# Kernel tuning notes

Hardware: AMD Instinct MI355X
Metric: run time of the kernel (lower is better)

## Reference

```python
import jax, jax.numpy as jnp
import numpy as np

N_NODES = 50000
N_EDGES = 1600000
F_IN = 128
C = 64          # block in/out channels
EF = 64         # edge MLP hidden dim
BLOCKS = 3
MLP_DIM = 128
N_CLASSES = 10
N_GRAPHS = 512
EPS = 1e-5


def setup_inputs() -> dict:
    key = jax.random.key(0)
    ks = jax.random.split(key, 32)
    s = 0.05
    inp = {
        "x": jax.random.normal(ks[0], (N_NODES, F_IN), jnp.float32),
        "edge_index": jax.random.randint(ks[1], (2, N_EDGES), 0, N_NODES, jnp.int64),
        "batch": jnp.sort(jax.random.randint(ks[2], (N_NODES,), 0, N_GRAPHS, jnp.int64)),
        "fc0_w": jax.random.normal(ks[3], (F_IN, C), jnp.float32) * s,
        "fc0_b": jnp.zeros((C,), jnp.float32),
        "fc1_w": jax.random.normal(ks[4], (BLOCKS * C, MLP_DIM), jnp.float32) * s,
        "fc1_b": jnp.zeros((MLP_DIM,), jnp.float32),
        "fc2_w": jax.random.normal(ks[5], (MLP_DIM, N_CLASSES), jnp.float32) * s,
        "fc2_b": jnp.zeros((N_CLASSES,), jnp.float32),
    }
    for i in range(BLOCKS):
        k = 6 + 4 * i
        inp[f"bn_g{i}"] = jnp.ones((C,), jnp.float32)
        inp[f"bn_b{i}"] = jnp.zeros((C,), jnp.float32)
        inp[f"w1_{i}"] = jax.random.normal(ks[k], (2 * C, EF), jnp.float32) * s
        inp[f"b1_{i}"] = jnp.zeros((EF,), jnp.float32)
        inp[f"w2_{i}"] = jax.random.normal(ks[k + 1], (EF, C), jnp.float32) * s
        inp[f"b2_{i}"] = jnp.zeros((C,), jnp.float32)
    return inp


def _batchnorm(x, g, b):
    mu = jnp.mean(x, axis=0)
    var = jnp.var(x, axis=0)
    return (x - mu) * jax.lax.rsqrt(var + EPS) * g + b


def _edge_conv(x, src, dst, w1, b1, w2, b2):
    # PyG-style EdgeConv: msg = MLP(concat[x_i, x_j - x_i]), max-aggregate at i
    xi = x[dst]                                  # [E, C]
    xj = x[src]                                  # [E, C]
    h = jax.nn.relu(jnp.concatenate([xi, xj - xi], axis=-1) @ w1 + b1)  # [E, EF]
    m = h @ w2 + b2                              # [E, C]
    agg = jax.ops.segment_max(m, dst, num_segments=N_NODES)
    return jnp.where(jnp.isfinite(agg), agg, 0.0)


def reference(x, edge_index, batch, fc0_w, fc0_b, fc1_w, fc1_b, fc2_w, fc2_b,
              bn_g0, bn_b0, w1_0, b1_0, w2_0, b2_0,
              bn_g1, bn_b1, w1_1, b1_1, w2_1, b2_1,
              bn_g2, bn_b2, w1_2, b1_2, w2_2, b2_2):
    src, dst = edge_index[0], edge_index[1]
    h = x @ fc0_w + fc0_b                        # [N, C]
    blocks = [(bn_g0, bn_b0, w1_0, b1_0, w2_0, b2_0),
              (bn_g1, bn_b1, w1_1, b1_1, w2_1, b2_1),
              (bn_g2, bn_b2, w1_2, b1_2, w2_2, b2_2)]
    xs = []
    for (g, b, w1, b1, w2, b2) in blocks:
        h = _batchnorm(h, g, b)
        h = jax.nn.relu(_edge_conv(h, src, dst, w1, b1, w2, b2))
        xs.append(h)
    cat = jnp.concatenate(xs, axis=-1)           # [N, 3C]
    # global mean pool over graphs
    sums = jax.ops.segment_sum(cat, batch, num_segments=N_GRAPHS)
    cnt = jax.ops.segment_sum(jnp.ones((N_NODES,), cat.dtype), batch,
                              num_segments=N_GRAPHS)
    pooled = sums / jnp.maximum(cnt, 1.0)[:, None]   # [G, 3C]
    hid = jax.nn.relu(pooled @ fc1_w + fc1_b)
    return jax.nn.log_softmax(hid @ fc2_w + fc2_b, axis=-1)
```

## Files before the change

### kernel.cpp

```cpp
#include <hip/hip_runtime.h>
#include <math.h>

#define N_NODES 50000
#define N_TILES 3125
#define N_EDGES 1600000
#define F_IN 128
#define C 64
#define EF 64
#define N_GRAPHS 512
#define MLP_DIM 128
#define N_CLASSES 10
#define EPS 1e-5f
#define NB 196
#define CAPB 16384
#define CHUNK 4096
#define NPASS1 391
#define NFC0 782
#define NSLICE 8
#define EDGE_GRID 2048

typedef __attribute__((ext_vector_type(8))) _Float16 half8;
typedef __attribute__((ext_vector_type(2))) _Float16 half2v;
typedef __attribute__((ext_vector_type(4))) float floatx4;
typedef __attribute__((ext_vector_type(4))) unsigned uintx4;

union Uh { uintx4 v; half2v h[4]; half8 h8; };

__device__ __forceinline__ unsigned short f2h(float a) {
    union { _Float16 f; unsigned short u; } c;
    c.f = (_Float16)a;
    return c.u;
}
__device__ __forceinline__ float h2f(unsigned short u) {
    union { unsigned short u; _Float16 f; } c;
    c.u = u;
    return (float)c.f;
}
__device__ __forceinline__ half2v pk2(float a, float b) {
    auto t = __builtin_amdgcn_cvt_pkrtz(a, b);
    union { decltype(t) i; half2v o; } c;
    c.i = t;
    return c.o;
}

__global__ __launch_bounds__(256, 3) void fc0_pass1_kernel(
        const int* __restrict__ src, const int* __restrict__ dst,
        int* __restrict__ gcur, unsigned* __restrict__ keys,
        const float* __restrict__ x, const float* __restrict__ w,
        const float* __restrict__ b, unsigned short* __restrict__ h0,
        float* __restrict__ bns) {
    __shared__ int lcnt[NB], lbase[NB], lcnt2[NB];
    __shared__ float bl1[4][64], bl2[4][64];
    int tid = threadIdx.x;

    if (blockIdx.x < NPASS1) {
        int e0 = blockIdx.x * CHUNK;
        unsigned k[CHUNK / 256];
        int bk[CHUNK / 256];
        for (int i = tid; i < NB; i += 256) lcnt[i] = 0;
        __syncthreads();
#pragma unroll
        for (int i = 0; i < CHUNK / 256; i++) {
            int e = e0 + i * 256 + tid;
            if (e < N_EDGES) {
                int d = dst[e];
                k[i] = ((unsigned)d << 16) | (unsigned)src[e];
                bk[i] = d >> 8;
                atomicAdd(&lcnt[bk[i]], 1);
            } else bk[i] = -1;
        }
        __syncthreads();
        for (int i = tid; i < NB; i += 256) {
            int c = lcnt[i];
            lbase[i] = c ? atomicAdd(&gcur[i], c) : 0;
            lcnt2[i] = 0;
        }
        __syncthreads();
#pragma unroll
        for (int i = 0; i < CHUNK / 256; i++) {
            if (bk[i] >= 0) {
                int r = atomicAdd(&lcnt2[bk[i]], 1);
                keys[(size_t)bk[i] * CAPB + lbase[bk[i]] + r] = k[i];
            }
        }
        return;
    }

    int bid = blockIdx.x - NPASS1;
    int lane = tid & 63, wid = tid >> 6;
    int q = lane >> 4, cl = lane & 15, kq = q * 8;

    Uh wf[4][4];
#pragma unroll
    for (int kh = 0; kh < 4; kh++)
#pragma unroll
        for (int cb = 0; cb < 4; cb++)
#pragma unroll
            for (int j = 0; j < 4; j++) {
                int k0 = kh * 32 + kq + 2 * j;
                int col = cb * 16 + cl;
                wf[kh][cb].h[j] = pk2(w[k0 * 64 + col], w[(k0 + 1) * 64 + col]);
            }
    float bv[4];
#pragma unroll
    for (int cb = 0; cb < 4; cb++) bv[cb] = b[cb * 16 + cl];
    float s1[4] = {0, 0, 0, 0}, s2[4] = {0, 0, 0, 0};

    for (int t = bid * 4 + wid; t < N_TILES; t += NFC0 * 4) {
        int nb = t * 16;
        floatx4 acc[4] = {{0,0,0,0},{0,0,0,0},{0,0,0,0},{0,0,0,0}};
#pragma unroll
        for (int kh = 0; kh < 4; kh++) {
            const float* xr = x + (size_t)(nb + cl) * F_IN + kh * 32 + kq;
            floatx4 xa = *(const floatx4*)xr;
            floatx4 xb = *(const floatx4*)(xr + 4);
            Uh xf;
            xf.h[0] = pk2(xa.x, xa.y); xf.h[1] = pk2(xa.z, xa.w);
            xf.h[2] = pk2(xb.x, xb.y); xf.h[3] = pk2(xb.z, xb.w);
#pragma unroll
            for (int cb = 0; cb < 4; cb++)
                acc[cb] = __builtin_amdgcn_mfma_f32_16x16x32_f16(xf.h8, wf[kh][cb].h8, acc[cb], 0, 0, 0);
        }
#pragma unroll
        for (int cb = 0; cb < 4; cb++)
#pragma unroll
            for (int r = 0; r < 4; r++) {
                float v = acc[cb][r] + bv[cb];
                h0[(size_t)(nb + q * 4 + r) * 64 + cb * 16 + cl] = f2h(v);
                s1[cb] += v; s2[cb] += v * v;
            }
    }
#pragma unroll
    for (int cb = 0; cb < 4; cb++) {
        s1[cb] += __shfl_xor(s1[cb], 16); s1[cb] += __shfl_xor(s1[cb], 32);
        s2[cb] += __shfl_xor(s2[cb], 16); s2[cb] += __shfl_xor(s2[cb], 32);
    }
    if (lane < 16) {
#pragma unroll
        for (int cb = 0; cb < 4; cb++) { bl1[wid][cb * 16 + lane] = s1[cb]; bl2[wid][cb * 16 + lane] = s2[cb]; }
    }
    __syncthreads();
    if (tid < 64) {
        float a  = bl1[0][tid] + bl1[1][tid] + bl1[2][tid] + bl1[3][tid];
        float c2 = bl2[0][tid] + bl2[1][tid] + bl2[2][tid] + bl2[3][tid];
        int sl = bid & (NSLICE - 1);
        atomicAdd(&bns[sl * 128 + tid], a);
        atomicAdd(&bns[sl * 128 + 64 + tid], c2);
    }
}

__device__ __forceinline__ void ab_body(int bid, int tid,
                                        const unsigned short* __restrict__ h,
                                        const float* __restrict__ bns,
                                        const float* __restrict__ g,
                                        const float* __restrict__ bb,
                                        const float* __restrict__ w1,
                                        const float* __restrict__ b1,
                                        unsigned short* __restrict__ A,
                                        unsigned short* __restrict__ Bb,
                                        float* scale, float* shift, float* cab) {
    int lane = tid & 63, wid = tid >> 6;
    int q = lane >> 4, cl = lane & 15, kq = q * 8;

    if (tid < 64) {
        float s1v = 0.f, s2v = 0.f;
#pragma unroll
        for (int s = 0; s < NSLICE; s++) { s1v += bns[s * 128 + tid]; s2v += bns[s * 128 + 64 + tid]; }
        float mu  = s1v * (1.0f / N_NODES);
        float var = s2v * (1.0f / N_NODES) - mu * mu;
        float sc  = g[tid] * rsqrtf(var + EPS);
        scale[tid] = sc;
        shift[tid] = bb[tid] - mu * sc;
    }
    __syncthreads();
    if (tid < 128) {
        int j = tid & 63;
        float acc = (tid < 64) ? b1[j] : 0.f;
        for (int k = 0; k < 64; k++) {
            float wa_ = w1[k * EF + j], wb_ = w1[(64 + k) * EF + j];
            acc = fmaf(shift[k], (tid < 64) ? (wa_ - wb_) : wb_, acc);
        }
        cab[tid] = acc;
    }
    Uh wa[2][4], wb[2][4];
#pragma unroll
    for (int kh = 0; kh < 2; kh++)
#pragma unroll
        for (int cb = 0; cb < 4; cb++)
#pragma unroll
            for (int j = 0; j < 4; j++) {
                int k0 = kh * 32 + kq + 2 * j;
                int col = cb * 16 + cl;
                float sa = scale[k0], sb = scale[k0 + 1];
                float a0 = w1[k0 * EF + col], b0 = w1[(64 + k0) * EF + col];
                float a1 = w1[(k0 + 1) * EF + col], b1v = w1[(64 + k0 + 1) * EF + col];
                wa[kh][cb].h[j] = pk2(sa * (a0 - b0), sb * (a1 - b1v));
                wb[kh][cb].h[j] = pk2(sa * b0, sb * b1v);
            }
    __syncthreads();
    float cav[4], cbv[4];
#pragma unroll
    for (int cb = 0; cb < 4; cb++) { cav[cb] = cab[cb * 16 + cl]; cbv[cb] = cab[64 + cb * 16 + cl]; }

    for (int t = bid * 4 + wid; t < N_TILES; t += NFC0 * 4) {
        int nb = t * 16;
        const unsigned short* hrow = h + (size_t)(nb + cl) * 64 + kq;
        Uh h0f, h1f;
        h0f.v = *(const uintx4*)hrow;
        h1f.v = *(const uintx4*)(hrow + 32);
        floatx4 accA[4] = {{0,0,0,0},{0,0,0,0},{0,0,0,0},{0,0,0,0}};
        floatx4 accB[4] = {{0,0,0,0},{0,0,0,0},{0,0,0,0},{0,0,0,0}};
#pragma unroll
        for (int cb = 0; cb < 4; cb++) {
            accA[cb] = __builtin_amdgcn_mfma_f32_16x16x32_f16(h0f.h8, wa[0][cb].h8, accA[cb], 0, 0, 0);
            accB[cb] = __builtin_amdgcn_mfma_f32_16x16x32_f16(h0f.h8, wb[0][cb].h8, accB[cb], 0, 0, 0);
            accA[cb] = __builtin_amdgcn_mfma_f32_16x16x32_f16(h1f.h8, wa[1][cb].h8, accA[cb], 0, 0, 0);
            accB[cb] = __builtin_amdgcn_mfma_f32_16x16x32_f16(h1f.h8, wb[1][cb].h8, accB[cb], 0, 0, 0);
        }
#pragma unroll
        for (int cb = 0; cb < 4; cb++)
#pragma unroll
            for (int r = 0; r < 4; r++) {
                size_t o = (size_t)(nb + q * 4 + r) * 64 + cb * 16 + cl;
                A[o]  = f2h(accA[cb][r] + cav[cb]);
                Bb[o] = f2h(accB[cb][r] + cbv[cb]);
            }
    }
}

__global__ __launch_bounds__(256, 4) void sort2_ab_kernel(
        const unsigned* __restrict__ keys, const int* __restrict__ bcnt,
        int* __restrict__ cnt, int* __restrict__ gtotal,
        int* __restrict__ row_start, unsigned short* __restrict__ sorted_src,
        const unsigned short* __restrict__ h, const float* __restrict__ bns,
        const float* __restrict__ g, const float* __restrict__ bb,
        const float* __restrict__ w1, const float* __restrict__ b1,
        unsigned short* __restrict__ A, unsigned short* __restrict__ Bb) {
    __shared__ int lc[256], loc[256], rs[256], cur[256];
    __shared__ int base;
    __shared__ float scale[64], shift[64], cab[128];
    int tid = threadIdx.x;
    if (blockIdx.x < NB) {
        int b = blockIdx.x;
        lc[tid] = 0;
        cur[tid] = 0;
        __syncthreads();
        int beg = b * CAPB, end = beg + bcnt[b];
        const unsigned* kb = keys + beg;
        int nk = end - beg;
        for (int p = tid; p < nk; p += 256)
            atomicAdd(&lc[(kb[p] >> 16) & 255], 1);
        __syncthreads();
        int node = b * 256 + tid;
        int c = lc[tid];
        if (node < N_NODES) cnt[node] = c;
        int pc = (c + 15) & ~15;
        loc[tid] = pc;
        __syncthreads();
        for (int off = 1; off < 256; off <<= 1) {
            int t = (tid >= off) ? loc[tid - off] : 0;
            __syncthreads();
            loc[tid] += t;
            __syncthreads();
        }
        if (tid == 255) base = atomicAdd(gtotal, loc[255]);
        __syncthreads();
        int myrs = base + loc[tid] - pc;
        rs[tid] = myrs;
        if (node < N_NODES) row_start[node] = myrs;
        __syncthreads();
        for (int p = tid; p < nk; p += 256) {
            unsigned k = kb[p];
            int lidx = (k >> 16) & 255;
            int r = atomicAdd(&cur[lidx], 1);
            sorted_src[rs[lidx] + r] = (unsigned short)(k & 0xFFFFu);
        }
        __syncthreads();
        if (node < N_NODES && c > 0) {
            unsigned short s0 = sorted_src[myrs];
            int pe = myrs + pc;
            for (int p = myrs + c; p < pe; p++) sorted_src[p] = s0;
        }
        return;
    }
    ab_body(blockIdx.x - NB, tid, h, bns, g, bb, w1, b1, A, Bb, scale, shift, cab);
}

__global__ __launch_bounds__(256, 4) void ab_mfma_kernel(
        const unsigned short* __restrict__ h, const float* __restrict__ bns,
        const float* __restrict__ g, const float* __restrict__ bb,
        const float* __restrict__ w1, const float* __restrict__ b1,
        unsigned short* __restrict__ A, unsigned short* __restrict__ Bb) {
    __shared__ float scale[64], shift[64], cab[128];
    ab_body(blockIdx.x, threadIdx.x, h, bns, g, bb, w1, b1, A, Bb, scale, shift, cab);
}

__global__ __launch_bounds__(256, 4) void edge_mfma_kernel(
        const unsigned short* __restrict__ A, const unsigned short* __restrict__ Bb,
        const int* __restrict__ row_start, const int* __restrict__ cnt,
        const unsigned short* __restrict__ sorted_src,
        const float* __restrict__ w2, const float* __restrict__ b2,
        unsigned short* __restrict__ catp, float* __restrict__ bnsNext) {
    __shared__ float r1[4][64], r2[4][64];
    int tid = threadIdx.x, lane = tid & 63, wid = tid >> 6;
    int kq = (lane >> 4) * 8;
    int cl = lane & 15;

    Uh bfr[2][4];
#pragma unroll
    for (int kh = 0; kh < 2; kh++)
#pragma unroll
        for (int cb = 0; cb < 4; cb++)
#pragma unroll
            for (int j = 0; j < 4; j++) {
                _Float16 w0 = (_Float16)w2[(kh * 32 + kq + 2 * j) * 64 + cb * 16 + cl];
                _Float16 w1v = (_Float16)w2[(kh * 32 + kq + 2 * j + 1) * 64 + cb * 16 + cl];
                bfr[kh][cb].h[j] = half2v{w0, w1v};
            }
    float b2j = b2[lane];
    float s1 = 0.f, s2 = 0.f;
    const half2v zeroh = {(_Float16)0.f, (_Float16)0.f};

    for (int n = blockIdx.x * 4 + wid; n < N_NODES; n += gridDim.x * 4) {
        int beg = row_start[n];
        int end = beg + ((cnt[n] + 15) & ~15);
        const unsigned short* arow = A + (size_t)n * 64 + kq;
        Uh a0u, a1u;
        a0u.v = __builtin_nontemporal_load((const uintx4*)(arow));
        a1u.v = __builtin_nontemporal_load((const uintx4*)(arow + 32));
        floatx4 rmax0 = {-INFINITY, -INFINITY, -INFINITY, -INFINITY};
        floatx4 rmax1 = rmax0, rmax2 = rmax0, rmax3 = rmax0;

        auto tile = [&](uintx4 u0, uintx4 u1) {
            Uh b0u, b1u, f0, f1;
            b0u.v = u0; b1u.v = u1;
#pragma unroll
            for (int j = 0; j < 4; j++) {
                f0.h[j] = __builtin_elementwise_max(a0u.h[j] + b0u.h[j], zeroh);
                f1.h[j] = __builtin_elementwise_max(a1u.h[j] + b1u.h[j], zeroh);
            }
            floatx4 acc0 = {0.f, 0.f, 0.f, 0.f}, acc1 = acc0, acc2 = acc0, acc3 = acc0;
            acc0 = __builtin_amdgcn_mfma_f32_16x16x32_f16(f0.h8, bfr[0][0].h8, acc0, 0, 0, 0);
            acc1 = __builtin_amdgcn_mfma_f32_16x16x32_f16(f0.h8, bfr[0][1].h8, acc1, 0, 0, 0);
            acc2 = __builtin_amdgcn_mfma_f32_16x16x32_f16(f0.h8, bfr[0][2].h8, acc2, 0, 0, 0);
            acc3 = __builtin_amdgcn_mfma_f32_16x16x32_f16(f0.h8, bfr[0][3].h8, acc3, 0, 0, 0);
            acc0 = __builtin_amdgcn_mfma_f32_16x16x32_f16(f1.h8, bfr[1][0].h8, acc0, 0, 0, 0);
            acc1 = __builtin_amdgcn_mfma_f32_16x16x32_f16(f1.h8, bfr[1][1].h8, acc1, 0, 0, 0);
            acc2 = __builtin_amdgcn_mfma_f32_16x16x32_f16(f1.h8, bfr[1][2].h8, acc2, 0, 0, 0);
            acc3 = __builtin_amdgcn_mfma_f32_16x16x32_f16(f1.h8, bfr[1][3].h8, acc3, 0, 0, 0);
            rmax0 = __builtin_elementwise_max(rmax0, acc0);
            rmax1 = __builtin_elementwise_max(rmax1, acc1);
            rmax2 = __builtin_elementwise_max(rmax2, acc2);
            rmax3 = __builtin_elementwise_max(rmax3, acc3);
        };
        auto gather = [&](int p, uintx4& u0, uintx4& u1) {
            int srcm = __builtin_nontemporal_load(&sorted_src[p + cl]);
            const unsigned short* brow = Bb + (size_t)srcm * 64 + kq;
            u0 = *(const uintx4*)(brow);
            u1 = *(const uintx4*)(brow + 32);
        };

        int p0 = beg;
        for (; p0 + 32 <= end; p0 += 32) {
            uintx4 x0, x1, y0, y1;
            gather(p0, x0, x1);
            gather(p0 + 16, y0, y1);
            tile(x0, x1);
            tile(y0, y1);
        }
        if (p0 < end) {
            uintx4 x0, x1;
            gather(p0, x0, x1);
            tile(x0, x1);
        }

        float v0 = fmaxf(fmaxf(rmax0.x, rmax0.y), fmaxf(rmax0.z, rmax0.w));
        float v1 = fmaxf(fmaxf(rmax1.x, rmax1.y), fmaxf(rmax1.z, rmax1.w));
        float v2 = fmaxf(fmaxf(rmax2.x, rmax2.y), fmaxf(rmax2.z, rmax2.w));
        float v3 = fmaxf(fmaxf(rmax3.x, rmax3.y), fmaxf(rmax3.z, rmax3.w));
        v0 = fmaxf(v0, __shfl_xor(v0, 16)); v0 = fmaxf(v0, __shfl_xor(v0, 32));
        v1 = fmaxf(v1, __shfl_xor(v1, 16)); v1 = fmaxf(v1, __shfl_xor(v1, 32));
        v2 = fmaxf(v2, __shfl_xor(v2, 16)); v2 = fmaxf(v2, __shfl_xor(v2, 32));
        v3 = fmaxf(v3, __shfl_xor(v3, 16)); v3 = fmaxf(v3, __shfl_xor(v3, 32));
        float vs = (lane & 32) ? ((lane & 16) ? v3 : v2) : ((lane & 16) ? v1 : v0);
        float v = fmaxf(vs + b2j, 0.f);
        __builtin_nontemporal_store(f2h(v), &catp[(size_t)n * 64 + lane]);
        s1 += v; s2 += v * v;
    }

    if (bnsNext) {
        r1[wid][lane] = s1; r2[wid][lane] = s2;
        __syncthreads();
        if (tid < 64) {
            float a  = r1[0][tid] + r1[1][tid] + r1[2][tid] + r1[3][tid];
            float c2 = r2[0][tid] + r2[1][tid] + r2[2][tid] + r2[3][tid];
            int sl = blockIdx.x & (NSLICE - 1);
            atomicAdd(&bnsNext[sl * 128 + tid], a);
            atomicAdd(&bnsNext[sl * 128 + 64 + tid], c2);
        }
    }
}

__global__ __launch_bounds__(192) void poolhead_kernel(const unsigned short* __restrict__ cat0,
                                                       const unsigned short* __restrict__ cat1,
                                                       const unsigned short* __restrict__ cat2,
                                                       const int* __restrict__ batch,
                                                       const float* __restrict__ fc1w,
                                                       const float* __restrict__ fc1b,
                                                       const float* __restrict__ fc2w,
                                                       const float* __restrict__ fc2b,
                                                       float* __restrict__ out) {
    __shared__ int se[2];
    __shared__ float p[192];
    __shared__ float hid[128];
    __shared__ float z[10];
    __shared__ float lse;
    int g = blockIdx.x, tid = threadIdx.x;
    if (tid < 2) {
        int target = g + tid;
        int lo = 0, hi = N_NODES;
        while (lo < hi) { int mid = (lo + hi) >> 1; if (batch[mid] < target) lo = mid + 1; else hi = mid; }
        se[tid] = lo;
    }
    __syncthreads();
    int s = se[0], e = se[1];
    const unsigned short* plane = (tid < 64) ? cat0 : ((tid < 128) ? cat1 : cat2);
    int col = tid & 63;
    float a0 = 0.f, a1 = 0.f, a2 = 0.f, a3 = 0.f;
    int r = s;
    for (; r + 4 <= e; r += 4) {
        a0 += h2f(plane[(size_t)(r + 0) * 64 + col]);
        a1 += h2f(plane[(size_t)(r + 1) * 64 + col]);
        a2 += h2f(plane[(size_t)(r + 2) * 64 + col]);
        a3 += h2f(plane[(size_t)(r + 3) * 64 + col]);
    }
    for (; r < e; r++) a0 += h2f(plane[(size_t)r * 64 + col]);
    float acc = (a0 + a1) + (a2 + a3);
    float denom = (e > s) ? (float)(e - s) : 1.0f;
    p[tid] = acc / denom;
    __syncthreads();
    if (tid < MLP_DIM) {
        float a = fc1b[tid];
        for (int k = 0; k < 192; k++) a = fmaf(p[k], fc1w[k * 128 + tid], a);
        hid[tid] = fmaxf(a, 0.f);
    }
    __syncthreads();
    if (tid < N_CLASSES) {
        float a = fc2b[tid];
        for (int k = 0; k < 128; k++) a = fmaf(hid[k], fc2w[k * 10 + tid], a);
        z[tid] = a;
    }
    __syncthreads();
    if (tid == 0) {
        float m = z[0];
        for (int i = 1; i < 10; i++) m = fmaxf(m, z[i]);
        float sm = 0.f;
        for (int i = 0; i < 10; i++) sm += expf(z[i] - m);
        lse = m + logf(sm);
    }
    __syncthreads();
    if (tid < N_CLASSES) out[g * 10 + tid] = z[tid] - lse;
}

extern "C" void kernel_launch(void* const* d_in, const int* in_sizes, int n_in,
                              void* d_out, int out_size, void* d_ws, size_t ws_size,
                              hipStream_t stream) {
    (void)in_sizes; (void)n_in; (void)out_size; (void)ws_size;
    const float* x    = (const float*)d_in[0];
    const int*   ei   = (const int*)d_in[1];
    const int*   batch= (const int*)d_in[2];
    const float* fc0w = (const float*)d_in[3];
    const float* fc0b = (const float*)d_in[4];
    const float* fc1w = (const float*)d_in[5];
    const float* fc1b = (const float*)d_in[6];
    const float* fc2w = (const float*)d_in[7];
    const float* fc2b = (const float*)d_in[8];
    const int* src = ei;
    const int* dst = ei + N_EDGES;
    float* out = (float*)d_out;

    char* w = (char*)d_ws;
    size_t off = 0;
    auto alloc = [&](size_t bytes) -> void* {
        void* p = w + off;
        off = (off + bytes + 255) & ~(size_t)255;
        return p;
    };
    const size_t MAX_PAD_EDGES = (size_t)N_EDGES + 16 * (size_t)N_NODES;

    const size_t BNS_OFF = 1280;
    const size_t ZBYTES  = BNS_OFF + 3 * NSLICE * 128 * 4;
    char* zbase = (char*)alloc(ZBYTES);
    int*   gcur   = (int*)zbase;
    int*   gtotal = (int*)(zbase + 1024);
    float* bnsAll = (float*)(zbase + BNS_OFF);

    unsigned short* cat0 = (unsigned short*)alloc((size_t)N_NODES * 64 * 2);
    unsigned short* cat1 = (unsigned short*)alloc((size_t)N_NODES * 64 * 2);
    unsigned short* cat2 = (unsigned short*)alloc((size_t)N_NODES * 64 * 2);
    unsigned short* h0   = (unsigned short*)alloc((size_t)N_NODES * 64 * 2);
    unsigned short* Ae   = (unsigned short*)alloc((size_t)N_NODES * 64 * 2);
    unsigned short* Be   = (unsigned short*)alloc((size_t)N_NODES * 64 * 2);
    unsigned* keys = (unsigned*)alloc((size_t)NB * CAPB * 4);
    unsigned short* sorted_src = (unsigned short*)alloc(MAX_PAD_EDGES * 2);
    int*   cnt       = (int*)alloc((size_t)N_NODES * 4);
    int*   row_start = (int*)alloc((size_t)N_NODES * 4);

    (void)hipMemsetAsync(zbase, 0, ZBYTES, stream);

    fc0_pass1_kernel<<<NPASS1 + NFC0, 256, 0, stream>>>(src, dst, gcur, keys,
                                                        x, fc0w, fc0b, h0, bnsAll);
    sort2_ab_kernel<<<NB + NFC0, 256, 0, stream>>>(
        keys, gcur, cnt, gtotal, row_start, sorted_src,
        h0, bnsAll,
        (const float*)d_in[9], (const float*)d_in[10],
        (const float*)d_in[11], (const float*)d_in[12], Ae, Be);

    unsigned short* planes[3] = {cat0, cat1, cat2};
    for (int blk = 0; blk < 3; blk++) {
        const float* w2 = (const float*)d_in[13 + 6 * blk];
        const float* b2 = (const float*)d_in[14 + 6 * blk];
        if (blk > 0) {
            ab_mfma_kernel<<<NFC0, 256, 0, stream>>>(
                planes[blk - 1], bnsAll + blk * NSLICE * 128,
                (const float*)d_in[9 + 6 * blk], (const float*)d_in[10 + 6 * blk],
                (const float*)d_in[11 + 6 * blk], (const float*)d_in[12 + 6 * blk], Ae, Be);
        }
        edge_mfma_kernel<<<EDGE_GRID, 256, 0, stream>>>(
            Ae, Be, row_start, cnt, sorted_src, w2, b2, planes[blk],
            (blk < 2) ? (bnsAll + (blk + 1) * NSLICE * 128) : nullptr);
    }

    poolhead_kernel<<<N_GRAPHS, 192, 0, stream>>>(cat0, cat1, cat2, batch,
                                                  fc1w, fc1b, fc2w, fc2b, out);
}
```

Baseline: 389.1 us.

## Split edge CSR by source-index range to improve gather locality

The sort step now buckets each node's incoming edges into four sub-lists keyed by the high bits of the source index. The edge kernel walks all nodes once per source range, keeping per-node partial maxima in shared memory, so the concurrently gathered B rows fall in a narrower address window and get more cache reuse. In exchange there is more padding (up to 16 slots per node per range), four times the row_start/cnt metadata, extra loop passes with A reloads, and more shared-memory use per block.

```diff
diff --git a/kernel.cpp b/kernel.cpp
--- a/kernel.cpp
+++ b/kernel.cpp
@@ -18,6 +18,8 @@
 #define NFC0 782
 #define NSLICE 8
 #define EDGE_GRID 2048
+#define NRANGE 4
+#define RSHIFT 14
 
 typedef __attribute__((ext_vector_type(8))) _Float16 half8;
 typedef __attribute__((ext_vector_type(2))) _Float16 half2v;
@@ -230,60 +232,75 @@
 
 __global__ __launch_bounds__(256, 4) void sort2_ab_kernel(
         const unsigned* __restrict__ keys, const int* __restrict__ bcnt,
-        int* __restrict__ cnt, int* __restrict__ gtotal,
-        int* __restrict__ row_start, unsigned short* __restrict__ sorted_src,
+        int* __restrict__ cnt2, int* __restrict__ gtotal,
+        int* __restrict__ row_start2, unsigned short* __restrict__ sorted_src,
         const unsigned short* __restrict__ h, const float* __restrict__ bns,
         const float* __restrict__ g, const float* __restrict__ bb,
         const float* __restrict__ w1, const float* __restrict__ b1,
         unsigned short* __restrict__ A, unsigned short* __restrict__ Bb) {
-    __shared__ int lc[256], loc[256], rs[256], cur[256];
-    __shared__ int base;
-    __shared__ float scale[64], shift[64], cab[128];
+    __shared__ union {
+        struct { int lc[1024]; int loc[256]; int rs[1024]; int cur[1024]; int base; } s;
+        struct { float scale[64]; float shift[64]; float cab[128]; } a;
+    } sh;
     int tid = threadIdx.x;
     if (blockIdx.x < NB) {
         int b = blockIdx.x;
-        lc[tid] = 0;
-        cur[tid] = 0;
-        __syncthreads();
-        int beg = b * CAPB, end = beg + bcnt[b];
+#pragma unroll
+        for (int j = 0; j < 4; j++) { sh.s.lc[tid * 4 + j] = 0; sh.s.cur[tid * 4 + j] = 0; }
+        __syncthreads();
+        int beg = b * CAPB, nk = bcnt[b];
         const unsigned* kb = keys + beg;
-        int nk = end - beg;
-        for (int p = tid; p < nk; p += 256)
-            atomicAdd(&lc[(kb[p] >> 16) & 255], 1);
-        __syncthreads();
-        int node = b * 256 + tid;
-        int c = lc[tid];
-        if (node < N_NODES) cnt[node] = c;
-        int pc = (c + 15) & ~15;
-        loc[tid] = pc;
-        __syncthreads();
-        for (int off = 1; off < 256; off <<= 1) {
-            int t = (tid >= off) ? loc[tid - off] : 0;
-            __syncthreads();
-            loc[tid] += t;
-            __syncthreads();
-        }
-        if (tid == 255) base = atomicAdd(gtotal, loc[255]);
-        __syncthreads();
-        int myrs = base + loc[tid] - pc;
-        rs[tid] = myrs;
-        if (node < N_NODES) row_start[node] = myrs;
-        __syncthreads();
         for (int p = tid; p < nk; p += 256) {
             unsigned k = kb[p];
-            int lidx = (k >> 16) & 255;
-            int r = atomicAdd(&cur[lidx], 1);
-            sorted_src[rs[lidx] + r] = (unsigned short)(k & 0xFFFFu);
-        }
-        __syncthreads();
-        if (node < N_NODES && c > 0) {
-            unsigned short s0 = sorted_src[myrs];
-            int pe = myrs + pc;
-            for (int p = myrs + c; p < pe; p++) sorted_src[p] = s0;
+            int sub = (int)((((k >> 16) & 255u) << 2) | ((k & 0xFFFFu) >> RSHIFT));
+            atomicAdd(&sh.s.lc[sub], 1);
+        }
+        __syncthreads();
+        int node = b * 256 + tid;
+        int pc[4]; int tsum = 0;
+#pragma unroll
+        for (int j = 0; j < 4; j++) { int c = sh.s.lc[tid * 4 + j]; pc[j] = (c + 15) & ~15; tsum += pc[j]; }
+        sh.s.loc[tid] = tsum;
+        __syncthreads();
+        for (int off = 1; off < 256; off <<= 1) {
+            int t = (tid >= off) ? sh.s.loc[tid - off] : 0;
+            __syncthreads();
+            sh.s.loc[tid] += t;
+            __syncthreads();
+        }
+        if (tid == 255) sh.s.base = atomicAdd(gtotal, sh.s.loc[255]);
+        __syncthreads();
+        int off0 = sh.s.base + sh.s.loc[tid] - tsum;
+#pragma unroll
+        for (int j = 0; j < 4; j++) {
+            sh.s.rs[tid * 4 + j] = off0;
+            if (node < N_NODES) {
+                cnt2[j * N_NODES + node] = sh.s.lc[tid * 4 + j];
+                row_start2[j * N_NODES + node] = off0;
+            }
+            off0 += pc[j];
+        }
+        __syncthreads();
+        for (int p = tid; p < nk; p += 256) {
+            unsigned k = kb[p];
+            int sub = (int)((((k >> 16) & 255u) << 2) | ((k & 0xFFFFu) >> RSHIFT));
+            int r = atomicAdd(&sh.s.cur[sub], 1);
+            sorted_src[sh.s.rs[sub] + r] = (unsigned short)(k & 0xFFFFu);
+        }
+        __syncthreads();
+#pragma unroll
+        for (int j = 0; j < 4; j++) {
+            int c = sh.s.lc[tid * 4 + j];
+            if (node < N_NODES && c > 0) {
+                int myrs = sh.s.rs[tid * 4 + j];
+                unsigned short s0 = sorted_src[myrs];
+                int pe = myrs + pc[j];
+                for (int p = myrs + c; p < pe; p++) sorted_src[p] = s0;
+            }
         }
         return;
     }
-    ab_body(blockIdx.x - NB, tid, h, bns, g, bb, w1, b1, A, Bb, scale, shift, cab);
+    ab_body(blockIdx.x - NB, tid, h, bns, g, bb, w1, b1, A, Bb, sh.a.scale, sh.a.shift, sh.a.cab);
 }
 
 __global__ __launch_bounds__(256, 4) void ab_mfma_kernel(
@@ -297,11 +314,12 @@
 
 __global__ __launch_bounds__(256, 4) void edge_mfma_kernel(
         const unsigned short* __restrict__ A, const unsigned short* __restrict__ Bb,
-        const int* __restrict__ row_start, const int* __restrict__ cnt,
+        const int* __restrict__ row_start2, const int* __restrict__ cnt2,
         const unsigned short* __restrict__ sorted_src,
         const float* __restrict__ w2, const float* __restrict__ b2,
         unsigned short* __restrict__ catp, float* __restrict__ bnsNext) {
     __shared__ float r1[4][64], r2[4][64];
+    __shared__ float pmax[4][7][64];
     int tid = threadIdx.x, lane = tid & 63, wid = tid >> 6;
     int kq = (lane >> 4) * 8;
     int cl = lane & 15;
@@ -317,73 +335,89 @@
                 _Float16 w1v = (_Float16)w2[(kh * 32 + kq + 2 * j + 1) * 64 + cb * 16 + cl];
                 bfr[kh][cb].h[j] = half2v{w0, w1v};
             }
+    const half2v zeroh = {(_Float16)0.f, (_Float16)0.f};
+
+#pragma unroll
+    for (int s = 0; s < 7; s++) pmax[wid][s][lane] = -INFINITY;
+
+    for (int r = 0; r < NRANGE; r++) {
+        const int* rsp = row_start2 + r * N_NODES;
+        const int* ctp = cnt2 + r * N_NODES;
+        int slot = 0;
+        for (int n = blockIdx.x * 4 + wid; n < N_NODES; n += gridDim.x * 4, slot++) {
+            int c = __builtin_nontemporal_load(ctp + n);
+            if (c == 0) continue;
+            int beg = __builtin_nontemporal_load(rsp + n);
+            int end = beg + ((c + 15) & ~15);
+            const unsigned short* arow = A + (size_t)n * 64 + kq;
+            Uh a0u, a1u;
+            a0u.v = __builtin_nontemporal_load((const uintx4*)(arow));
+            a1u.v = __builtin_nontemporal_load((const uintx4*)(arow + 32));
+            floatx4 rmax0 = {-INFINITY, -INFINITY, -INFINITY, -INFINITY};
+            floatx4 rmax1 = rmax0, rmax2 = rmax0, rmax3 = rmax0;
+
+            auto tile = [&](uintx4 u0, uintx4 u1) {
+                Uh b0u, b1u, f0, f1;
+                b0u.v = u0; b1u.v = u1;
+#pragma unroll
+                for (int j = 0; j < 4; j++) {
+                    f0.h[j] = __builtin_elementwise_max(a0u.h[j] + b0u.h[j], zeroh);
+                    f1.h[j] = __builtin_elementwise_max(a1u.h[j] + b1u.h[j], zeroh);
+                }
+                floatx4 acc0 = {0.f, 0.f, 0.f, 0.f}, acc1 = acc0, acc2 = acc0, acc3 = acc0;
+                acc0 = __builtin_amdgcn_mfma_f32_16x16x32_f16(f0.h8, bfr[0][0].h8, acc0, 0, 0, 0);
+                acc1 = __builtin_amdgcn_mfma_f32_16x16x32_f16(f0.h8, bfr[0][1].h8, acc1, 0, 0, 0);
+                acc2 = __builtin_amdgcn_mfma_f32_16x16x32_f16(f0.h8, bfr[0][2].h8, acc2, 0, 0, 0);
+                acc3 = __builtin_amdgcn_mfma_f32_16x16x32_f16(f0.h8, bfr[0][3].h8, acc3, 0, 0, 0);
+                acc0 = __builtin_amdgcn_mfma_f32_16x16x32_f16(f1.h8, bfr[1][0].h8, acc0, 0, 0, 0);
+                acc1 = __builtin_amdgcn_mfma_f32_16x16x32_f16(f1.h8, bfr[1][1].h8, acc1, 0, 0, 0);
+                acc2 = __builtin_amdgcn_mfma_f32_16x16x32_f16(f1.h8, bfr[1][2].h8, acc2, 0, 0, 0);
+                acc3 = __builtin_amdgcn_mfma_f32_16x16x32_f16(f1.h8, bfr[1][3].h8, acc3, 0, 0, 0);
+                rmax0 = __builtin_elementwise_max(rmax0, acc0);
+                rmax1 = __builtin_elementwise_max(rmax1, acc1);
+                rmax2 = __builtin_elementwise_max(rmax2, acc2);
+                rmax3 = __builtin_elementwise_max(rmax3, acc3);
+            };
+            auto gather = [&](int p, uintx4& u0, uintx4& u1) {
+                int srcm = __builtin_nontemporal_load(&sorted_src[p + cl]);
+                const unsigned short* brow = Bb + (size_t)srcm * 64 + kq;
+                u0 = *(const uintx4*)(brow);
+                u1 = *(const uintx4*)(brow + 32);
+            };
+
+            int p0 = beg;
+            for (; p0 + 32 <= end; p0 += 32) {
+                uintx4 x0, x1, y0, y1;
+                gather(p0, x0, x1);
+                gather(p0 + 16, y0, y1);
+                tile(x0, x1);
+                tile(y0, y1);
+            }
+            if (p0 < end) {
+                uintx4 x0, x1;
+                gather(p0, x0, x1);
+                tile(x0, x1);
+            }
+
+            float v0 = fmaxf(fmaxf(rmax0.x, rmax0.y), fmaxf(rmax0.z, rmax0.w));
+            float v1 = fmaxf(fmaxf(rmax1.x, rmax1.y), fmaxf(rmax1.z, rmax1.w));
+            float v2 = fmaxf(fmaxf(rmax2.x, rmax2.y), fmaxf(rmax2.z, rmax2.w));
+            float v3 = fmaxf(fmaxf(rmax3.x, rmax3.y), fmaxf(rmax3.z, rmax3.w));
+            v0 = fmaxf(v0, __shfl_xor(v0, 16)); v0 = fmaxf(v0, __shfl_xor(v0, 32));
+            v1 = fmaxf(v1, __shfl_xor(v1, 16)); v1 = fmaxf(v1, __shfl_xor(v1, 32));
+            v2 = fmaxf(v2, __shfl_xor(v2, 16)); v2 = fmaxf(v2, __shfl_xor(v2, 32));
+            v3 = fmaxf(v3, __shfl_xor(v3, 16)); v3 = fmaxf(v3, __shfl_xor(v3, 32));
+            float vs = (lane & 32) ? ((lane & 16) ? v3 : v2) : ((lane & 16) ? v1 : v0);
+            float* pm = &pmax[wid][slot][lane];
+            *pm = fmaxf(*pm, vs);
+        }
+    }
+
     float b2j = b2[lane];
     float s1 = 0.f, s2 = 0.f;
-    const half2v zeroh = {(_Float16)0.f, (_Float16)0.f};
-
-    for (int n = blockIdx.x * 4 + wid; n < N_NODES; n += gridDim.x * 4) {
-        int beg = row_start[n];
-        int end = beg + ((cnt[n] + 15) & ~15);
-        const unsigned short* arow = A + (size_t)n * 64 + kq;
-        Uh a0u, a1u;
-        a0u.v = __builtin_nontemporal_load((const uintx4*)(arow));
-        a1u.v = __builtin_nontemporal_load((const uintx4*)(arow + 32));
-        floatx4 rmax0 = {-INFINITY, -INFINITY, -INFINITY, -INFINITY};
-        floatx4 rmax1 = rmax0, rmax2 = rmax0, rmax3 = rmax0;
-
-        auto tile = [&](uintx4 u0, uintx4 u1) {
-            Uh b0u, b1u, f0, f1;
-            b0u.v = u0; b1u.v = u1;
-#pragma unroll
-            for (int j = 0; j < 4; j++) {
-                f0.h[j] = __builtin_elementwise_max(a0u.h[j] + b0u.h[j], zeroh);
-                f1.h[j] = __builtin_elementwise_max(a1u.h[j] + b1u.h[j], zeroh);
-            }
-            floatx4 acc0 = {0.f, 0.f, 0.f, 0.f}, acc1 = acc0, acc2 = acc0, acc3 = acc0;
-            acc0 = __builtin_amdgcn_mfma_f32_16x16x32_f16(f0.h8, bfr[0][0].h8, acc0, 0, 0, 0);
-            acc1 = __builtin_amdgcn_mfma_f32_16x16x32_f16(f0.h8, bfr[0][1].h8, acc1, 0, 0, 0);
-            acc2 = __builtin_amdgcn_mfma_f32_16x16x32_f16(f0.h8, bfr[0][2].h8, acc2, 0, 0, 0);
-            acc3 = __builtin_amdgcn_mfma_f32_16x16x32_f16(f0.h8, bfr[0][3].h8, acc3, 0, 0, 0);
-            acc0 = __builtin_amdgcn_mfma_f32_16x16x32_f16(f1.h8, bfr[1][0].h8, acc0, 0, 0, 0);
-            acc1 = __builtin_amdgcn_mfma_f32_16x16x32_f16(f1.h8, bfr[1][1].h8, acc1, 0, 0, 0);
-            acc2 = __builtin_amdgcn_mfma_f32_16x16x32_f16(f1.h8, bfr[1][2].h8, acc2, 0, 0, 0);
-            acc3 = __builtin_amdgcn_mfma_f32_16x16x32_f16(f1.h8, bfr[1][3].h8, acc3, 0, 0, 0);
-            rmax0 = __builtin_elementwise_max(rmax0, acc0);
-            rmax1 = __builtin_elementwise_max(rmax1, acc1);
-            rmax2 = __builtin_elementwise_max(rmax2, acc2);
-            rmax3 = __builtin_elementwise_max(rmax3, acc3);
-        };
-        auto gather = [&](int p, uintx4& u0, uintx4& u1) {
-            int srcm = __builtin_nontemporal_load(&sorted_src[p + cl]);
-            const unsigned short* brow = Bb + (size_t)srcm * 64 + kq;
-            u0 = *(const uintx4*)(brow);
-            u1 = *(const uintx4*)(brow + 32);
-        };
-
-        int p0 = beg;
-        for (; p0 + 32 <= end; p0 += 32) {
-            uintx4 x0, x1, y0, y1;
-            gather(p0, x0, x1);
-            gather(p0 + 16, y0, y1);
-            tile(x0, x1);
-            tile(y0, y1);
-        }
-        if (p0 < end) {
-            uintx4 x0, x1;
-            gather(p0, x0, x1);
-            tile(x0, x1);
-        }
-
-        float v0 = fmaxf(fmaxf(rmax0.x, rmax0.y), fmaxf(rmax0.z, rmax0.w));
-        float v1 = fmaxf(fmaxf(rmax1.x, rmax1.y), fmaxf(rmax1.z, rmax1.w));
-        float v2 = fmaxf(fmaxf(rmax2.x, rmax2.y), fmaxf(rmax2.z, rmax2.w));
-        float v3 = fmaxf(fmaxf(rmax3.x, rmax3.y), fmaxf(rmax3.z, rmax3.w));
-        v0 = fmaxf(v0, __shfl_xor(v0, 16)); v0 = fmaxf(v0, __shfl_xor(v0, 32));
-        v1 = fmaxf(v1, __shfl_xor(v1, 16)); v1 = fmaxf(v1, __shfl_xor(v1, 32));
-        v2 = fmaxf(v2, __shfl_xor(v2, 16)); v2 = fmaxf(v2, __shfl_xor(v2, 32));
-        v3 = fmaxf(v3, __shfl_xor(v3, 16)); v3 = fmaxf(v3, __shfl_xor(v3, 32));
-        float vs = (lane & 32) ? ((lane & 16) ? v3 : v2) : ((lane & 16) ? v1 : v0);
-        float v = fmaxf(vs + b2j, 0.f);
+    int slot = 0;
+    for (int n = blockIdx.x * 4 + wid; n < N_NODES; n += gridDim.x * 4, slot++) {
+        float v = fmaxf(pmax[wid][slot][lane] + b2j, 0.f);
         __builtin_nontemporal_store(f2h(v), &catp[(size_t)n * 64 + lane]);
         s1 += v; s2 += v * v;
     }
@@ -486,7 +520,7 @@
         off = (off + bytes + 255) & ~(size_t)255;
         return p;
     };
-    const size_t MAX_PAD_EDGES = (size_t)N_EDGES + 16 * (size_t)N_NODES;
+    const size_t MAX_PAD_EDGES = (size_t)N_EDGES + 16 * (size_t)NRANGE * (size_t)N_NODES;
 
     const size_t BNS_OFF = 1280;
     const size_t ZBYTES  = BNS_OFF + 3 * NSLICE * 128 * 4;
@@ -503,15 +537,15 @@
     unsigned short* Be   = (unsigned short*)alloc((size_t)N_NODES * 64 * 2);
     unsigned* keys = (unsigned*)alloc((size_t)NB * CAPB * 4);
     unsigned short* sorted_src = (unsigned short*)alloc(MAX_PAD_EDGES * 2);
-    int*   cnt       = (int*)alloc((size_t)N_NODES * 4);
-    int*   row_start = (int*)alloc((size_t)N_NODES * 4);
+    int*   cnt2       = (int*)alloc((size_t)NRANGE * N_NODES * 4);
+    int*   row_start2 = (int*)alloc((size_t)NRANGE * N_NODES * 4);
 
     (void)hipMemsetAsync(zbase, 0, ZBYTES, stream);
 
     fc0_pass1_kernel<<<NPASS1 + NFC0, 256, 0, stream>>>(src, dst, gcur, keys,
                                                         x, fc0w, fc0b, h0, bnsAll);
     sort2_ab_kernel<<<NB + NFC0, 256, 0, stream>>>(
-        keys, gcur, cnt, gtotal, row_start, sorted_src,
+        keys, gcur, cnt2, gtotal, row_start2, sorted_src,
         h0, bnsAll,
         (const float*)d_in[9], (const float*)d_in[10],
         (const float*)d_in[11], (const float*)d_in[12], Ae, Be);
@@ -527,7 +561,7 @@
                 (const float*)d_in[11 + 6 * blk], (const float*)d_in[12 + 6 * blk], Ae, Be);
         }
         edge_mfma_kernel<<<EDGE_GRID, 256, 0, stream>>>(
-            Ae, Be, row_start, cnt, sorted_src, w2, b2, planes[blk],
+            Ae, Be, row_start2, cnt2, sorted_src, w2, b2, planes[blk],
             (blk < 2) ? (bnsAll + (blk + 1) * NSLICE * 128) : nullptr);
     }
 
```

Result: slower. 585.0 us (+50.3%).
